# Kernel tuning notes

Measured on AMD Instinct MI355X. Metric: run time of the kernel, lower is better.

Reference implementation:

```python
import jax, jax.numpy as jnp
import numpy as np
from math import sqrt

B, T, I, H, O, R = 128, 1000, 3, 512, 1, 2
NOISE_STD = 0.05
ALPHA = 0.2


def setup_inputs() -> dict:
    key = jax.random.key(0)
    ks = jax.random.split(key, 6)
    inp = jax.random.normal(ks[0], (B, T, I), dtype=jnp.float32)
    noise = jax.random.normal(ks[1], (B, T, H), dtype=jnp.float32)
    # parameters initialized as in the torch module
    wi = jax.random.normal(ks[2], (I, H), dtype=jnp.float32)
    si = jnp.ones((I,), dtype=jnp.float32)
    m = jax.random.normal(ks[3], (H, R), dtype=jnp.float32) * (1.0 / sqrt(H))
    n = jax.random.normal(ks[4], (H, R), dtype=jnp.float32) * (1.0 / sqrt(H))
    wo = jax.random.normal(ks[5], (H, O), dtype=jnp.float32) * (2.0 / H)
    so = jnp.ones((O,), dtype=jnp.float32)
    h0 = jnp.zeros((H,), dtype=jnp.float32)
    return {"input": inp, "noise": noise, "wi": wi, "si": si, "m": m,
            "n": n, "wo": wo, "so": so, "h0": h0}


def reference(input, noise, wi, si, m, n, wo, so, h0):
    # proxy parameters: wi_full = (wi.T * si).T, wo_full = wo * so
    wi_full = si[:, None] * wi          # (I, H)
    wo_full = wo * so                   # (H, O)
    batch = input.shape[0]
    h_init = jnp.broadcast_to(h0, (batch, h0.shape[0]))  # (B, H)

    def step(h, xs):
        x_t, z_t = xs                   # (B, I), (B, H)
        r = jnp.tanh(h)
        rec = (r @ n) @ m.T             # low-rank recurrence, (B, H)
        h_new = h + NOISE_STD * z_t + ALPHA * (-h + rec + x_t @ wi_full)
        out = jnp.tanh(h_new) @ wo_full  # (B, O)
        return h_new, (out, h_new)

    xs = (jnp.swapaxes(input, 0, 1), jnp.swapaxes(noise, 0, 1))  # time-major
    _, (outs, hs) = jax.lax.scan(step, h_init, xs)
    output = jnp.swapaxes(outs, 0, 1)               # (B, T, O)
    trajectories = jnp.concatenate(
        [h_init[:, None, :], jnp.swapaxes(hs, 0, 1)], axis=1)  # (B, T+1, H)
    return output, trajectories
```

## Files before the change

### kernel.cpp

```cpp
#include <hip/hip_runtime.h>
#include <stdint.h>

#define B_ 128
#define T_ 1000
#define H_ 512
#define PH 8
#define NPHASE 125

typedef float vfloat4 __attribute__((ext_vector_type(4)));

template <int CTRL>
__device__ __forceinline__ float dpp_add(float x) {
    int moved = __builtin_amdgcn_update_dpp(0, __float_as_int(x), CTRL, 0xf, 0xf, true);
    return x + __int_as_float(moved);
}

__device__ __forceinline__ void wave_reduce3(float& p0, float& p1, float& p2) {
    p0 = dpp_add<0x111>(p0); p1 = dpp_add<0x111>(p1); p2 = dpp_add<0x111>(p2);
    p0 = dpp_add<0x112>(p0); p1 = dpp_add<0x112>(p1); p2 = dpp_add<0x112>(p2);
    p0 = dpp_add<0x114>(p0); p1 = dpp_add<0x114>(p1); p2 = dpp_add<0x114>(p2);
    p0 = dpp_add<0x118>(p0); p1 = dpp_add<0x118>(p1); p2 = dpp_add<0x118>(p2);
    p0 = dpp_add<0x142>(p0); p1 = dpp_add<0x142>(p1); p2 = dpp_add<0x142>(p2);
    p0 = dpp_add<0x143>(p0); p1 = dpp_add<0x143>(p1); p2 = dpp_add<0x143>(p2);
}

__device__ __forceinline__ float fast_tanh(float x) {
    float E = __builtin_amdgcn_exp2f(x * 2.885390081777927f);
    float r = __builtin_amdgcn_rcpf(E + 1.0f);
    return __builtin_fmaf(-2.0f, r, 1.0f);
}

__global__ __launch_bounds__(128, 1) void lowrank_rnn_kernel(
    const float* __restrict__ input,
    const float* __restrict__ noise,
    const float* __restrict__ wi,
    const float* __restrict__ si,
    const float* __restrict__ m,
    const float* __restrict__ n,
    const float* __restrict__ wo,
    const float* __restrict__ so,
    const float* __restrict__ h0,
    float* __restrict__ out)
{
    const int b    = blockIdx.x;
    const int tid  = threadIdx.x;
    const int wid  = tid >> 6;
    const int lane = tid & 63;
    const int j0   = lane * 8;

    __shared__ __align__(16) vfloat4 ub[2][PH][2][64];
    __shared__ float os[T_ + 1];
    __shared__ int   flags[2];

    if (tid == 0) { flags[0] = 0; flags[1] = 0; }
    __syncthreads();
    volatile int* vprod = &flags[0];
    volatile int* vcons = &flags[1];

    if (wid == 1) {
        float wS0[8], wS1[8], wS2[8];
        #pragma unroll
        for (int i = 0; i < 3; ++i) {
            float s = 0.2f * si[i];
            float* dst = (i == 0) ? wS0 : (i == 1) ? wS1 : wS2;
            #pragma unroll
            for (int q = 0; q < 2; ++q) {
                vfloat4 vw = *(const vfloat4*)(wi + i * H_ + j0 + 4 * q);
                dst[4*q] = vw.x * s; dst[4*q+1] = vw.y * s;
                dst[4*q+2] = vw.z * s; dst[4*q+3] = vw.w * s;
            }
        }
        const float* zb = noise + (size_t)b * T_ * H_ + j0;
        const float* xb = input + (size_t)b * T_ * 3;

        for (int p = 0; p < NPHASE; ++p) {
            if (p >= 2) {
                while (*vcons < p - 1) {}
                asm volatile("" ::: "memory");
            }
            const int half = p & 1;
            #pragma unroll
            for (int s = 0; s < PH; ++s) {
                const int t = p * PH + s;
                vfloat4 zl = *(const vfloat4*)(zb + (size_t)t * H_);
                vfloat4 zh = *(const vfloat4*)(zb + (size_t)t * H_ + 4);
                float x0 = xb[3*t], x1 = xb[3*t+1], x2 = xb[3*t+2];
                float zz[8] = {zl.x, zl.y, zl.z, zl.w, zh.x, zh.y, zh.z, zh.w};
                float u[8];
                #pragma unroll
                for (int k = 0; k < 8; ++k) {
                    float xw = __builtin_fmaf(x0, wS0[k],
                               __builtin_fmaf(x1, wS1[k], x2 * wS2[k]));
                    u[k] = __builtin_fmaf(zz[k], 0.05f, xw);
                }
                vfloat4 ulo = {u[0], u[1], u[2], u[3]};
                vfloat4 uhi = {u[4], u[5], u[6], u[7]};
                ub[half][s][0][lane] = ulo;
                ub[half][s][1][lane] = uhi;
            }
            asm volatile("s_waitcnt lgkmcnt(0)" ::: "memory");
            if (lane == 0) *vprod = p + 1;
        }
    } else {
        float h[8], n0[8], n1[8], m0S[8], m1S[8], wof[8];
        {
            const float so0 = so[0];
            const float* nb = n + 2 * j0;
            const float* mb = m + 2 * j0;
            #pragma unroll
            for (int q = 0; q < 4; ++q) {
                vfloat4 vn = *(const vfloat4*)(nb + 4 * q);
                n0[2*q] = vn.x; n1[2*q] = vn.y; n0[2*q+1] = vn.z; n1[2*q+1] = vn.w;
                vfloat4 vm = *(const vfloat4*)(mb + 4 * q);
                m0S[2*q] = 0.2f * vm.x;   m1S[2*q] = 0.2f * vm.y;
                m0S[2*q+1] = 0.2f * vm.z; m1S[2*q+1] = 0.2f * vm.w;
            }
            #pragma unroll
            for (int q = 0; q < 2; ++q) {
                vfloat4 vw = *(const vfloat4*)(wo + j0 + 4 * q);
                wof[4*q] = vw.x * so0; wof[4*q+1] = vw.y * so0;
                wof[4*q+2] = vw.z * so0; wof[4*q+3] = vw.w * so0;
                vfloat4 vh = *(const vfloat4*)(h0 + j0 + 4 * q);
                h[4*q] = vh.x; h[4*q+1] = vh.y; h[4*q+2] = vh.z; h[4*q+3] = vh.w;
            }
        }
        float* trajBase = out + (size_t)B_ * T_ + (size_t)b * (T_ + 1) * H_;
        {
            vfloat4 lo = {h[0], h[1], h[2], h[3]};
            vfloat4 hi = {h[4], h[5], h[6], h[7]};
            *(vfloat4*)(trajBase + j0)     = lo;
            *(vfloat4*)(trajBase + j0 + 4) = hi;
        }

        for (int p = 0; p < NPHASE; ++p) {
            while (*vprod < p + 1) {}
            asm volatile("" ::: "memory");
            const int half = p & 1;
            #pragma unroll
            for (int s = 0; s < PH; ++s) {
                const int t = p * PH + s;
                vfloat4 ulo = ub[half][s][0][lane];
                vfloat4 uhi = ub[half][s][1][lane];

                float r[8];
                #pragma unroll
                for (int k = 0; k < 8; ++k) r[k] = fast_tanh(h[k]);

                float p0 = r[0] * n0[0], p1 = r[0] * n1[0], p2 = r[0] * wof[0];
                #pragma unroll
                for (int k = 1; k < 8; ++k) {
                    p0 = __builtin_fmaf(r[k], n0[k], p0);
                    p1 = __builtin_fmaf(r[k], n1[k], p1);
                    p2 = __builtin_fmaf(r[k], wof[k], p2);
                }
                wave_reduce3(p0, p1, p2);

                float uu[8] = {ulo.x, ulo.y, ulo.z, ulo.w, uhi.x, uhi.y, uhi.z, uhi.w};
                float base[8];
                #pragma unroll
                for (int k = 0; k < 8; ++k)
                    base[k] = __builtin_fmaf(h[k], 0.8f, uu[k]);

                float a0 = __int_as_float(__builtin_amdgcn_readlane(__float_as_int(p0), 63));
                float a1 = __int_as_float(__builtin_amdgcn_readlane(__float_as_int(p1), 63));
                if (lane == 63) os[t] = p2;

                #pragma unroll
                for (int k = 0; k < 8; ++k)
                    h[k] = __builtin_fmaf(a0, m0S[k], __builtin_fmaf(a1, m1S[k], base[k]));

                float* tr = trajBase + (size_t)(t + 1) * H_ + j0;
                vfloat4 lo = {h[0], h[1], h[2], h[3]};
                vfloat4 hi = {h[4], h[5], h[6], h[7]};
                *(vfloat4*)tr       = lo;
                *(vfloat4*)(tr + 4) = hi;
            }
            asm volatile("s_waitcnt lgkmcnt(0)" ::: "memory");
            if (lane == 0) *vcons = p + 1;
        }

        {
            float r[8];
            #pragma unroll
            for (int k = 0; k < 8; ++k) r[k] = fast_tanh(h[k]);
            float p2 = r[0] * wof[0];
            #pragma unroll
            for (int k = 1; k < 8; ++k) p2 = __builtin_fmaf(r[k], wof[k], p2);
            p2 = dpp_add<0x111>(p2); p2 = dpp_add<0x112>(p2);
            p2 = dpp_add<0x114>(p2); p2 = dpp_add<0x118>(p2);
            p2 = dpp_add<0x142>(p2); p2 = dpp_add<0x143>(p2);
            if (lane == 63) os[T_] = p2;
        }
        float* outp = out + (size_t)b * T_;
        for (int idx = lane; idx < T_; idx += 64)
            outp[idx] = os[idx + 1];
    }
}

extern "C" void kernel_launch(void* const* d_in, const int* in_sizes, int n_in,
                              void* d_out, int out_size, void* d_ws, size_t ws_size,
                              hipStream_t stream) {
    const float* input = (const float*)d_in[0];
    const float* noise = (const float*)d_in[1];
    const float* wi    = (const float*)d_in[2];
    const float* si    = (const float*)d_in[3];
    const float* m     = (const float*)d_in[4];
    const float* n     = (const float*)d_in[5];
    const float* wo    = (const float*)d_in[6];
    const float* so    = (const float*)d_in[7];
    const float* h0    = (const float*)d_in[8];
    float* out = (float*)d_out;

    hipLaunchKernelGGL(lowrank_rnn_kernel, dim3(B_), dim3(128), 0, stream,
                       input, noise, wi, si, m, n, wo, so, h0, out);
}
```

Before: 290.3 us.

## Offload output projection and trajectory stores to producer wave via LDS

```diff
diff --git a/kernel.cpp b/kernel.cpp
--- a/kernel.cpp
+++ b/kernel.cpp
@@ -15,13 +15,19 @@
     return x + __int_as_float(moved);
 }
 
-__device__ __forceinline__ void wave_reduce3(float& p0, float& p1, float& p2) {
-    p0 = dpp_add<0x111>(p0); p1 = dpp_add<0x111>(p1); p2 = dpp_add<0x111>(p2);
-    p0 = dpp_add<0x112>(p0); p1 = dpp_add<0x112>(p1); p2 = dpp_add<0x112>(p2);
-    p0 = dpp_add<0x114>(p0); p1 = dpp_add<0x114>(p1); p2 = dpp_add<0x114>(p2);
-    p0 = dpp_add<0x118>(p0); p1 = dpp_add<0x118>(p1); p2 = dpp_add<0x118>(p2);
-    p0 = dpp_add<0x142>(p0); p1 = dpp_add<0x142>(p1); p2 = dpp_add<0x142>(p2);
-    p0 = dpp_add<0x143>(p0); p1 = dpp_add<0x143>(p1); p2 = dpp_add<0x143>(p2);
+__device__ __forceinline__ void wave_reduce2(float& p0, float& p1) {
+    p0 = dpp_add<0x111>(p0); p1 = dpp_add<0x111>(p1);
+    p0 = dpp_add<0x112>(p0); p1 = dpp_add<0x112>(p1);
+    p0 = dpp_add<0x114>(p0); p1 = dpp_add<0x114>(p1);
+    p0 = dpp_add<0x118>(p0); p1 = dpp_add<0x118>(p1);
+    p0 = dpp_add<0x142>(p0); p1 = dpp_add<0x142>(p1);
+    p0 = dpp_add<0x143>(p0); p1 = dpp_add<0x143>(p1);
+}
+
+__device__ __forceinline__ float wave_reduce1(float p) {
+    p = dpp_add<0x111>(p); p = dpp_add<0x112>(p); p = dpp_add<0x114>(p);
+    p = dpp_add<0x118>(p); p = dpp_add<0x142>(p); p = dpp_add<0x143>(p);
+    return p;
 }
 
 __device__ __forceinline__ float fast_tanh(float x) {
@@ -49,6 +55,9 @@
     const int j0   = lane * 8;
 
     __shared__ __align__(16) vfloat4 ub[2][PH][2][64];
+    __shared__ __align__(16) vfloat4 rb[2][PH][2][64];
+    __shared__ __align__(16) vfloat4 hb[2][PH][2][64];
+    __shared__ __align__(16) vfloat4 rfin[2][64];
     __shared__ float os[T_ + 1];
     __shared__ int   flags[2];
 
@@ -58,34 +67,83 @@
     volatile int* vcons = &flags[1];
 
     if (wid == 1) {
-        float wS0[8], wS1[8], wS2[8];
-        #pragma unroll
-        for (int i = 0; i < 3; ++i) {
-            float s = 0.2f * si[i];
-            float* dst = (i == 0) ? wS0 : (i == 1) ? wS1 : wS2;
+        float wS0[8], wS1[8], wS2[8], wof[8];
+        {
+            const float so0 = so[0];
+            #pragma unroll
+            for (int i = 0; i < 3; ++i) {
+                float s = 0.2f * si[i];
+                float* dst = (i == 0) ? wS0 : (i == 1) ? wS1 : wS2;
+                #pragma unroll
+                for (int q = 0; q < 2; ++q) {
+                    vfloat4 vw = *(const vfloat4*)(wi + i * H_ + j0 + 4 * q);
+                    dst[4*q] = vw.x * s; dst[4*q+1] = vw.y * s;
+                    dst[4*q+2] = vw.z * s; dst[4*q+3] = vw.w * s;
+                }
+            }
             #pragma unroll
             for (int q = 0; q < 2; ++q) {
-                vfloat4 vw = *(const vfloat4*)(wi + i * H_ + j0 + 4 * q);
-                dst[4*q] = vw.x * s; dst[4*q+1] = vw.y * s;
-                dst[4*q+2] = vw.z * s; dst[4*q+3] = vw.w * s;
+                vfloat4 vw = *(const vfloat4*)(wo + j0 + 4 * q);
+                wof[4*q] = vw.x * so0; wof[4*q+1] = vw.y * so0;
+                wof[4*q+2] = vw.z * so0; wof[4*q+3] = vw.w * so0;
             }
         }
         const float* zb = noise + (size_t)b * T_ * H_ + j0;
         const float* xb = input + (size_t)b * T_ * 3;
-
-        for (int p = 0; p < NPHASE; ++p) {
-            if (p >= 2) {
-                while (*vcons < p - 1) {}
+        float* trajBase = out + (size_t)B_ * T_ + (size_t)b * (T_ + 1) * H_;
+
+        {
+            vfloat4 a = *(const vfloat4*)(h0 + j0);
+            vfloat4 c = *(const vfloat4*)(h0 + j0 + 4);
+            *(vfloat4*)(trajBase + j0)     = a;
+            *(vfloat4*)(trajBase + j0 + 4) = c;
+        }
+
+        auto emit_phase = [&](int pp) {
+            const int hf = pp & 1;
+            #pragma unroll
+            for (int s = 0; s < PH; ++s) {
+                const int t = pp * PH + s;
+                vfloat4 rl = rb[hf][s][0][lane];
+                vfloat4 rh = rb[hf][s][1][lane];
+                float p2 = rl.x * wof[0];
+                p2 = __builtin_fmaf(rl.y, wof[1], p2);
+                p2 = __builtin_fmaf(rl.z, wof[2], p2);
+                p2 = __builtin_fmaf(rl.w, wof[3], p2);
+                p2 = __builtin_fmaf(rh.x, wof[4], p2);
+                p2 = __builtin_fmaf(rh.y, wof[5], p2);
+                p2 = __builtin_fmaf(rh.z, wof[6], p2);
+                p2 = __builtin_fmaf(rh.w, wof[7], p2);
+                p2 = wave_reduce1(p2);
+                if (lane == 63) os[t] = p2;
+                vfloat4 hl = hb[hf][s][0][lane];
+                vfloat4 hh = hb[hf][s][1][lane];
+                float* tr = trajBase + (size_t)(t + 1) * H_ + j0;
+                *(vfloat4*)tr       = hl;
+                *(vfloat4*)(tr + 4) = hh;
+            }
+        };
+
+        for (int q = 0; q < NPHASE; ++q) {
+            if (q >= 2) {
+                while (*vcons < q - 1) {}
                 asm volatile("" ::: "memory");
             }
-            const int half = p & 1;
-            #pragma unroll
-            for (int s = 0; s < PH; ++s) {
-                const int t = p * PH + s;
-                vfloat4 zl = *(const vfloat4*)(zb + (size_t)t * H_);
-                vfloat4 zh = *(const vfloat4*)(zb + (size_t)t * H_ + 4);
+            vfloat4 zl[PH], zh[PH];
+            #pragma unroll
+            for (int s = 0; s < PH; ++s) {
+                const float* g = zb + (size_t)(q * PH + s) * H_;
+                zl[s] = *(const vfloat4*)g;
+                zh[s] = *(const vfloat4*)(g + 4);
+            }
+            if (q >= 2) emit_phase(q - 2);
+            const int half = q & 1;
+            #pragma unroll
+            for (int s = 0; s < PH; ++s) {
+                const int t = q * PH + s;
                 float x0 = xb[3*t], x1 = xb[3*t+1], x2 = xb[3*t+2];
-                float zz[8] = {zl.x, zl.y, zl.z, zl.w, zh.x, zh.y, zh.z, zh.w};
+                float zz[8] = {zl[s].x, zl[s].y, zl[s].z, zl[s].w,
+                               zh[s].x, zh[s].y, zh[s].z, zh[s].w};
                 float u[8];
                 #pragma unroll
                 for (int k = 0; k < 8; ++k) {
@@ -99,12 +157,34 @@
                 ub[half][s][1][lane] = uhi;
             }
             asm volatile("s_waitcnt lgkmcnt(0)" ::: "memory");
-            if (lane == 0) *vprod = p + 1;
-        }
+            if (lane == 0) *vprod = q + 1;
+        }
+        while (*vcons < NPHASE) {}
+        asm volatile("" ::: "memory");
+        emit_phase(NPHASE - 2);
+        emit_phase(NPHASE - 1);
+        while (*vcons < NPHASE + 1) {}
+        asm volatile("" ::: "memory");
+        {
+            vfloat4 rl = rfin[0][lane], rh = rfin[1][lane];
+            float p2 = rl.x * wof[0];
+            p2 = __builtin_fmaf(rl.y, wof[1], p2);
+            p2 = __builtin_fmaf(rl.z, wof[2], p2);
+            p2 = __builtin_fmaf(rl.w, wof[3], p2);
+            p2 = __builtin_fmaf(rh.x, wof[4], p2);
+            p2 = __builtin_fmaf(rh.y, wof[5], p2);
+            p2 = __builtin_fmaf(rh.z, wof[6], p2);
+            p2 = __builtin_fmaf(rh.w, wof[7], p2);
+            p2 = wave_reduce1(p2);
+            if (lane == 63) os[T_] = p2;
+        }
+        asm volatile("s_waitcnt lgkmcnt(0)" ::: "memory");
+        float* outp = out + (size_t)b * T_;
+        for (int idx = lane; idx < T_; idx += 64)
+            outp[idx] = os[idx + 1];
     } else {
-        float h[8], n0[8], n1[8], m0S[8], m1S[8], wof[8];
-        {
-            const float so0 = so[0];
+        float h[8], n0[8], n1[8], m0S[8], m1S[8];
+        {
             const float* nb = n + 2 * j0;
             const float* mb = m + 2 * j0;
             #pragma unroll
@@ -117,45 +197,37 @@
             }
             #pragma unroll
             for (int q = 0; q < 2; ++q) {
-                vfloat4 vw = *(const vfloat4*)(wo + j0 + 4 * q);
-                wof[4*q] = vw.x * so0; wof[4*q+1] = vw.y * so0;
-                wof[4*q+2] = vw.z * so0; wof[4*q+3] = vw.w * so0;
                 vfloat4 vh = *(const vfloat4*)(h0 + j0 + 4 * q);
                 h[4*q] = vh.x; h[4*q+1] = vh.y; h[4*q+2] = vh.z; h[4*q+3] = vh.w;
             }
-        }
-        float* trajBase = out + (size_t)B_ * T_ + (size_t)b * (T_ + 1) * H_;
-        {
-            vfloat4 lo = {h[0], h[1], h[2], h[3]};
-            vfloat4 hi = {h[4], h[5], h[6], h[7]};
-            *(vfloat4*)(trajBase + j0)     = lo;
-            *(vfloat4*)(trajBase + j0 + 4) = hi;
         }
 
         for (int p = 0; p < NPHASE; ++p) {
             while (*vprod < p + 1) {}
             asm volatile("" ::: "memory");
             const int half = p & 1;
-            #pragma unroll
-            for (int s = 0; s < PH; ++s) {
-                const int t = p * PH + s;
-                vfloat4 ulo = ub[half][s][0][lane];
-                vfloat4 uhi = ub[half][s][1][lane];
-
+            vfloat4 cul = ub[half][0][0][lane];
+            vfloat4 cuh = ub[half][0][1][lane];
+            #pragma unroll
+            for (int s = 0; s < PH; ++s) {
+                vfloat4 nul, nuh;
+                if (s < PH - 1) {
+                    nul = ub[half][s+1][0][lane];
+                    nuh = ub[half][s+1][1][lane];
+                }
                 float r[8];
                 #pragma unroll
                 for (int k = 0; k < 8; ++k) r[k] = fast_tanh(h[k]);
 
-                float p0 = r[0] * n0[0], p1 = r[0] * n1[0], p2 = r[0] * wof[0];
+                float p0 = r[0] * n0[0], p1 = r[0] * n1[0];
                 #pragma unroll
                 for (int k = 1; k < 8; ++k) {
                     p0 = __builtin_fmaf(r[k], n0[k], p0);
                     p1 = __builtin_fmaf(r[k], n1[k], p1);
-                    p2 = __builtin_fmaf(r[k], wof[k], p2);
-                }
-                wave_reduce3(p0, p1, p2);
-
-                float uu[8] = {ulo.x, ulo.y, ulo.z, ulo.w, uhi.x, uhi.y, uhi.z, uhi.w};
+                }
+                wave_reduce2(p0, p1);
+
+                float uu[8] = {cul.x, cul.y, cul.z, cul.w, cuh.x, cuh.y, cuh.z, cuh.w};
                 float base[8];
                 #pragma unroll
                 for (int k = 0; k < 8; ++k)
@@ -163,37 +235,36 @@
 
                 float a0 = __int_as_float(__builtin_amdgcn_readlane(__float_as_int(p0), 63));
                 float a1 = __int_as_float(__builtin_amdgcn_readlane(__float_as_int(p1), 63));
-                if (lane == 63) os[t] = p2;
 
                 #pragma unroll
                 for (int k = 0; k < 8; ++k)
                     h[k] = __builtin_fmaf(a0, m0S[k], __builtin_fmaf(a1, m1S[k], base[k]));
 
-                float* tr = trajBase + (size_t)(t + 1) * H_ + j0;
-                vfloat4 lo = {h[0], h[1], h[2], h[3]};
-                vfloat4 hi = {h[4], h[5], h[6], h[7]};
-                *(vfloat4*)tr       = lo;
-                *(vfloat4*)(tr + 4) = hi;
+                vfloat4 rlo = {r[0], r[1], r[2], r[3]};
+                vfloat4 rhi = {r[4], r[5], r[6], r[7]};
+                rb[half][s][0][lane] = rlo;
+                rb[half][s][1][lane] = rhi;
+                vfloat4 hlo = {h[0], h[1], h[2], h[3]};
+                vfloat4 hhi = {h[4], h[5], h[6], h[7]};
+                hb[half][s][0][lane] = hlo;
+                hb[half][s][1][lane] = hhi;
+
+                cul = nul; cuh = nuh;
             }
             asm volatile("s_waitcnt lgkmcnt(0)" ::: "memory");
             if (lane == 0) *vcons = p + 1;
         }
-
-        {
-            float r[8];
-            #pragma unroll
-            for (int k = 0; k < 8; ++k) r[k] = fast_tanh(h[k]);
-            float p2 = r[0] * wof[0];
-            #pragma unroll
-            for (int k = 1; k < 8; ++k) p2 = __builtin_fmaf(r[k], wof[k], p2);
-            p2 = dpp_add<0x111>(p2); p2 = dpp_add<0x112>(p2);
-            p2 = dpp_add<0x114>(p2); p2 = dpp_add<0x118>(p2);
-            p2 = dpp_add<0x142>(p2); p2 = dpp_add<0x143>(p2);
-            if (lane == 63) os[T_] = p2;
-        }
-        float* outp = out + (size_t)b * T_;
-        for (int idx = lane; idx < T_; idx += 64)
-            outp[idx] = os[idx + 1];
+        while (*vprod < NPHASE) {}
+        asm volatile("" ::: "memory");
+        float r[8];
+        #pragma unroll
+        for (int k = 0; k < 8; ++k) r[k] = fast_tanh(h[k]);
+        vfloat4 rlo = {r[0], r[1], r[2], r[3]};
+        vfloat4 rhi = {r[4], r[5], r[6], r[7]};
+        rfin[0][lane] = rlo;
+        rfin[1][lane] = rhi;
+        asm volatile("s_waitcnt lgkmcnt(0)" ::: "memory");
+        if (lane == 0) *vcons = NPHASE + 1;
     }
 }
 
```

Result: no change. 295.8 us (+1.9%).
